# Optimization experiments

Measured on AMD Instinct MI355X. Metric: run time of the kernel, lower is better.

The kernel has to match this reference:

```python
import jax, jax.numpy as jnp
import numpy as np

EPS = 1e-9  # Dice BatchNormalization epsilon


def dice(x, alpha):
    # Keras BatchNormalization(axis=-1, center=False, scale=False) in training
    # mode: normalize over all axes except the last using batch statistics.
    mean = jnp.mean(x, axis=(0, 1), keepdims=True)
    var = jnp.var(x, axis=(0, 1), keepdims=True)
    x_normed = (x - mean) * jax.lax.rsqrt(var + EPS)
    p = jax.nn.sigmoid(x_normed)
    return alpha * (1.0 - p) * x + p * x


def setup_inputs() -> dict:
    key = jax.random.key(0)
    ks = jax.random.split(key, 11)
    B, T, D = 512, 2048, 20
    keys_ = jax.random.normal(ks[0], (B, T, D), dtype=jnp.float32)
    query = jax.random.normal(ks[1], (B, 1, D), dtype=jnp.float32)
    mask = jax.random.randint(ks[2], (B, T), 0, 2) > 0
    # DNN tower weights: hidden dims 80 -> 32 -> 16, attention head 16 -> 1
    W0 = jax.random.normal(ks[3], (80, 32), dtype=jnp.float32) * 0.1
    b0 = jax.random.normal(ks[4], (32,), dtype=jnp.float32) * 0.1
    a0 = jax.random.normal(ks[5], (32,), dtype=jnp.float32) * 0.1
    W1 = jax.random.normal(ks[6], (32, 16), dtype=jnp.float32) * 0.1
    b1 = jax.random.normal(ks[7], (16,), dtype=jnp.float32) * 0.1
    a1 = jax.random.normal(ks[8], (16,), dtype=jnp.float32) * 0.1
    wk = jax.random.normal(ks[9], (16, 1), dtype=jnp.float32) * 0.1
    bk = jax.random.normal(ks[10], (1,), dtype=jnp.float32) * 0.1
    return {"keys": keys_, "query": query, "mask": mask,
            "W0": W0, "b0": b0, "a0": a0,
            "W1": W1, "b1": b1, "a1": a1,
            "wk": wk, "bk": bk}


def reference(keys, query, mask, W0, b0, a0, W1, b1, a1, wk, bk):
    B, T, D = keys.shape
    # repeat query along the key/time axis: [B,1,D] -> [B,T,D]
    queries = jnp.broadcast_to(query, (B, T, D))
    # local-activation features: [B,T,4D] = [B,T,80]
    att = jnp.concatenate([queries, keys, queries - keys, queries * keys], axis=-1)
    # DNN tower with Dice activations (dropout is identity at inference)
    h = dice(att @ W0 + b0, a0)   # [B,T,32]
    h = dice(h @ W1 + b1, a1)     # [B,T,16]
    score = h @ wk + bk           # [B,T,1]
    outputs = jnp.transpose(score, (0, 2, 1))  # [B,1,T]
    # NOTE: the original code computes the masked scores into self.outputs but
    # then (weight_normalization=False, return_score=False) overwrites it with
    # matmul(outputs, keys) using the UNMASKED scores -- we reproduce that.
    return jnp.matmul(outputs, keys)  # [B,1,D]
```

## Files before the change

### kernel.cpp

```cpp
#include <hip/hip_runtime.h>


#define BB 512
#define TT 2048
#define DD 20
#define C0 32
#define C1 16

#define NTH 256
#define NPOS 4
#define POSB (NTH * NPOS)
#define NSLOT 8

#define WS_P1 0
#define WS_P2 512
#define WS_SCALE0 768
#define WS_SHIFT0 800
#define WS_SCALE1 832
#define WS_SHIFT1 848
#define WS_ZERO_N 768
#define WS_BLOB 896
#define BLOB_J 24
#define BLOB_B (C0 * BLOB_J)

#define PIN(x) asm volatile("" : "+v"(x))

__device__ __forceinline__ float fast_sigmoid(float x) {
    return __builtin_amdgcn_rcpf(1.0f + __expf(-x));
}

__device__ __forceinline__ void load_krow(const float* __restrict__ row,
                                          float* kk) {
    const float4* kr = (const float4*)row;
    float4 a = kr[0], b = kr[1], c = kr[2], d = kr[3], e = kr[4];
    kk[0] = a.x; kk[1] = a.y; kk[2] = a.z; kk[3] = a.w;
    kk[4] = b.x; kk[5] = b.y; kk[6] = b.z; kk[7] = b.w;
    kk[8] = c.x; kk[9] = c.y; kk[10] = c.z; kk[11] = c.w;
    kk[12] = d.x; kk[13] = d.y; kk[14] = d.z; kk[15] = d.w;
    kk[16] = e.x; kk[17] = e.y; kk[18] = e.z; kk[19] = e.w;
}

__global__ void prep_kernel(const float* __restrict__ query,
                            const float* __restrict__ W0,
                            const float* __restrict__ b0,
                            float* __restrict__ blob) {
    const int b = blockIdx.x * 2 + (threadIdx.x >> 5);
    const int j = threadIdx.x & 31;
    float cj = b0[j];
    float* dst = blob + (size_t)b * BLOB_B + j * BLOB_J;
#pragma unroll
    for (int d = 0; d < DD; ++d) {
        float w_q = W0[d * C0 + j];
        float w_k = W0[(DD + d) * C0 + j];
        float w_d = W0[(2 * DD + d) * C0 + j];
        float w_p = W0[(3 * DD + d) * C0 + j];
        float qd = query[b * DD + d];
        dst[d] = w_k - w_d + qd * w_p;
        cj = fmaf(qd, w_q + w_d, cj);
    }
    dst[20] = cj;
}

__global__ __launch_bounds__(NTH, 2) void pass1_kernel(
    const float* __restrict__ keys, const float* __restrict__ blob,
    float* __restrict__ sums) {
    const int b = blockIdx.x;
    const int tid = threadIdx.x, lane = tid & 63;
    const float* bA = blob + (size_t)b * BLOB_B;
    const float* kbase = keys + (size_t)b * TT * DD;

    float s[C0], q[C0];
#pragma unroll
    for (int j = 0; j < C0; ++j) { s[j] = 0.f; q[j] = 0.f; }

#pragma unroll 1
    for (int r = 0; r < TT / POSB; ++r) {
        float kk[NPOS][DD];
#pragma unroll
        for (int pp = 0; pp < NPOS; ++pp)
            load_krow(kbase + (size_t)(r * POSB + tid + pp * NTH) * DD,
                      kk[pp]);
#pragma unroll
        for (int pp = 0; pp < NPOS; ++pp)
#pragma unroll
            for (int d = 0; d < DD; ++d) PIN(kk[pp][d]);
#pragma unroll
        for (int j = 0; j < C0; ++j) {
            const float* wr = bA + j * BLOB_J;
            const float cj = wr[20];
            float sv = 0.f, qv = 0.f;
#pragma unroll
            for (int pp = 0; pp < NPOS; ++pp) {
                float hh = cj;
#pragma unroll
                for (int d = 0; d < DD; ++d)
                    hh = fmaf(kk[pp][d], wr[d], hh);
                sv += hh;
                qv = fmaf(hh, hh, qv);
            }
            s[j] += sv;
            q[j] += qv;
        }
    }
    float redv = 0.f;
#pragma unroll
    for (int v = 0; v < 2 * C0; ++v) {
        float val = (v < C0) ? s[v] : q[v - C0];
#pragma unroll
        for (int o = 32; o >= 1; o >>= 1) val += __shfl_xor(val, o);
        if (lane == v) redv = val;
    }
    atomicAdd(&sums[WS_P1 + (blockIdx.x & (NSLOT - 1)) * (2 * C0) + lane],
              redv);
}

__global__ void finalize_kernel(float* __restrict__ ws, int nch, int srcOff,
                                int scOff, int shOff) {
    int j = threadIdx.x;
    if (j < nch) {
        float s = 0.f, q = 0.f;
#pragma unroll
        for (int k = 0; k < NSLOT; ++k) {
            s += ws[srcOff + k * 2 * nch + j];
            q += ws[srcOff + k * 2 * nch + nch + j];
        }
        const float invN = 1.0f / (float)(BB * TT);
        float mean = s * invN;
        float var = q * invN - mean * mean;
        float scv = rsqrtf(var + 1e-9f);
        ws[scOff + j] = scv;
        ws[shOff + j] = -mean * scv;
    }
}

#define LOAD_AND_PIN_KEYS()                                                  \
    const float* kbase = keys + ((size_t)b * TT + chunk * POSB) * DD;        \
    float kk[NPOS][DD];                                                      \
    _Pragma("unroll") for (int pp = 0; pp < NPOS; ++pp)                      \
        load_krow(kbase + (size_t)(tid + pp * NTH) * DD, kk[pp]);            \
    _Pragma("unroll") for (int pp = 0; pp < NPOS; ++pp)                      \
        _Pragma("unroll") for (int d = 0; d < DD; ++d) PIN(kk[pp][d]);

#define TOWER_JLOOP()                                                        \
    _Pragma("unroll 1") for (int j = 0; j < C0; ++j) {                       \
        const float* wr = bA + j * BLOB_J;                                   \
        const float* ur = W1 + j * C1;                                       \
        const float cj = wr[20];                                             \
        const float sc = stats[WS_SCALE0 + j];                               \
        const float sh = stats[WS_SHIFT0 + j];                               \
        const float al = a0[j];                                              \
        const float nal = 1.0f - al;                                         \
        float h[NPOS];                                                       \
        _Pragma("unroll") for (int pp = 0; pp < NPOS; ++pp) {                \
            float hh = cj;                                                   \
            _Pragma("unroll") for (int d = 0; d < DD; ++d)                   \
                hh = fmaf(kk[pp][d], wr[d], hh);                             \
            h[pp] = hh;                                                      \
        }                                                                    \
        _Pragma("unroll") for (int pp = 0; pp < NPOS; ++pp) {                \
            float pr = fast_sigmoid(fmaf(h[pp], sc, sh));                    \
            float h0d = h[pp] * fmaf(pr, nal, al);                           \
            _Pragma("unroll") for (int c = 0; c < C1; ++c)                   \
                h1[pp][c] = fmaf(h0d, ur[c], h1[pp][c]);                     \
        }                                                                    \
    }

__global__ __launch_bounds__(NTH, 2) void pass2_kernel(
    const float* __restrict__ keys, const float* __restrict__ blob,
    const float* __restrict__ a0, const float* __restrict__ W1,
    const float* __restrict__ b1, const float* __restrict__ stats,
    float* __restrict__ sums) {
    const int b = blockIdx.x >> 1, chunk = blockIdx.x & 1;
    const int tid = threadIdx.x, lane = tid & 63;
    const float* bA = blob + (size_t)b * BLOB_B;

    LOAD_AND_PIN_KEYS()

    float h1[NPOS][C1];
#pragma unroll
    for (int pp = 0; pp < NPOS; ++pp)
#pragma unroll
        for (int c = 0; c < C1; ++c) h1[pp][c] = 0.f;

    TOWER_JLOOP()

    float s1[C1], q1[C1];
#pragma unroll
    for (int c = 0; c < C1; ++c) {
        float bc = b1[c], sv = 0.f, qv = 0.f;
#pragma unroll
        for (int pp = 0; pp < NPOS; ++pp) {
            float v = h1[pp][c] + bc;
            sv += v;
            qv = fmaf(v, v, qv);
        }
        s1[c] = sv;
        q1[c] = qv;
    }
    float redv = 0.f;
#pragma unroll
    for (int v = 0; v < 2 * C1; ++v) {
        float val = (v < C1) ? s1[v] : q1[v - C1];
#pragma unroll
        for (int o = 32; o >= 1; o >>= 1) val += __shfl_xor(val, o);
        if (lane == v) redv = val;
    }
    if (lane < 2 * C1)
        atomicAdd(&sums[WS_P2 + (blockIdx.x & (NSLOT - 1)) * (2 * C1) + lane],
                  redv);
}

__global__ __launch_bounds__(NTH, 2) void pass3_kernel(
    const float* __restrict__ keys, const float* __restrict__ blob,
    const float* __restrict__ a0, const float* __restrict__ W1,
    const float* __restrict__ b1, const float* __restrict__ a1,
    const float* __restrict__ wk, const float* __restrict__ bk,
    const float* __restrict__ stats, float* __restrict__ out) {
    const int b = blockIdx.x >> 1, chunk = blockIdx.x & 1;
    const int tid = threadIdx.x, lane = tid & 63;
    const float* bA = blob + (size_t)b * BLOB_B;

    LOAD_AND_PIN_KEYS()

    float h1[NPOS][C1];
#pragma unroll
    for (int pp = 0; pp < NPOS; ++pp)
#pragma unroll
        for (int c = 0; c < C1; ++c) h1[pp][c] = 0.f;

    TOWER_JLOOP()

    const float bkv = bk[0];
    float oacc[DD];
#pragma unroll
    for (int d = 0; d < DD; ++d) oacc[d] = 0.f;
#pragma unroll
    for (int pp = 0; pp < NPOS; ++pp) {
        float score = bkv;
#pragma unroll
        for (int c = 0; c < C1; ++c) {
            float v = h1[pp][c] + b1[c];
            float pr = fast_sigmoid(
                fmaf(v, stats[WS_SCALE1 + c], stats[WS_SHIFT1 + c]));
            float al = a1[c];
            float hd = v * fmaf(pr, 1.0f - al, al);
            score = fmaf(hd, wk[c], score);
        }
#pragma unroll
        for (int d = 0; d < DD; ++d)
            oacc[d] = fmaf(score, kk[pp][d], oacc[d]);
    }
    float redv = 0.f;
#pragma unroll
    for (int v = 0; v < DD; ++v) {
        float val = oacc[v];
#pragma unroll
        for (int o = 32; o >= 1; o >>= 1) val += __shfl_xor(val, o);
        if (lane == v) redv = val;
    }
    if (lane < DD) atomicAdd(&out[b * DD + lane], redv);
}

extern "C" void kernel_launch(void* const* d_in, const int* in_sizes, int n_in,
                              void* d_out, int out_size, void* d_ws,
                              size_t ws_size, hipStream_t stream) {
    const float* keys = (const float*)d_in[0];
    const float* query = (const float*)d_in[1];
    const float* W0 = (const float*)d_in[3];
    const float* b0 = (const float*)d_in[4];
    const float* a0 = (const float*)d_in[5];
    const float* W1 = (const float*)d_in[6];
    const float* b1 = (const float*)d_in[7];
    const float* a1 = (const float*)d_in[8];
    const float* wk = (const float*)d_in[9];
    const float* bk = (const float*)d_in[10];
    float* out = (float*)d_out;
    float* ws = (float*)d_ws;
    float* blob = ws + WS_BLOB;

    hipMemsetAsync(ws, 0, WS_ZERO_N * sizeof(float), stream);
    hipMemsetAsync(out, 0, (size_t)out_size * sizeof(float), stream);

    prep_kernel<<<BB / 2, 64, 0, stream>>>(query, W0, b0, blob);

    pass1_kernel<<<BB, NTH, 0, stream>>>(keys, blob, ws);
    finalize_kernel<<<1, 32, 0, stream>>>(ws, C0, WS_P1, WS_SCALE0, WS_SHIFT0);
    pass2_kernel<<<BB * 2, NTH, 0, stream>>>(keys, blob, a0, W1, b1, ws, ws);
    finalize_kernel<<<1, 16, 0, stream>>>(ws, C1, WS_P2, WS_SCALE1, WS_SHIFT1);
    pass3_kernel<<<BB * 2, NTH, 0, stream>>>(keys, blob, a0, W1, b1, a1, wk,
                                             bk, ws, out);
}
```

Baseline: 279.9 us.

## Fuse three passes into one cooperative kernel with grid-wide syncs

Replaces the pass1/finalize/pass2/finalize/pass3 launch chain with a single cooperative kernel of one block per batch row. Grid-wide syncs separate the statistics phases, and each block finalizes the BN statistics into shared memory itself. The output is written directly after a block-level reduction, so the output memset and the atomics go away. Each block now walks all 2048 positions in every phase, which halves the grid for passes 2 and 3. The cooperative launch also needs all 512 blocks to be co-resident, with a fallback to separate kernels when they are not.

```diff
diff --git a/kernel.cpp b/kernel.cpp
--- a/kernel.cpp
+++ b/kernel.cpp
@@ -1,4 +1,7 @@
 #include <hip/hip_runtime.h>
+#include <hip/hip_cooperative_groups.h>
+
+namespace cg = cooperative_groups;
 
 
 #define BB 512
@@ -10,20 +13,19 @@
 #define NTH 256
 #define NPOS 4
 #define POSB (NTH * NPOS)
+#define NROUND (TT / POSB)
 #define NSLOT 8
 
 #define WS_P1 0
 #define WS_P2 512
-#define WS_SCALE0 768
-#define WS_SHIFT0 800
-#define WS_SCALE1 832
-#define WS_SHIFT1 848
 #define WS_ZERO_N 768
 #define WS_BLOB 896
 #define BLOB_J 24
 #define BLOB_B (C0 * BLOB_J)
 
 #define PIN(x) asm volatile("" : "+v"(x))
+#define AGLOAD(p) \
+    __hip_atomic_load((p), __ATOMIC_RELAXED, __HIP_MEMORY_SCOPE_AGENT)
 
 __device__ __forceinline__ float fast_sigmoid(float x) {
     return __builtin_amdgcn_rcpf(1.0f + __expf(-x));
@@ -61,83 +63,10 @@
     dst[20] = cj;
 }
 
-__global__ __launch_bounds__(NTH, 2) void pass1_kernel(
-    const float* __restrict__ keys, const float* __restrict__ blob,
-    float* __restrict__ sums) {
-    const int b = blockIdx.x;
-    const int tid = threadIdx.x, lane = tid & 63;
-    const float* bA = blob + (size_t)b * BLOB_B;
-    const float* kbase = keys + (size_t)b * TT * DD;
-
-    float s[C0], q[C0];
-#pragma unroll
-    for (int j = 0; j < C0; ++j) { s[j] = 0.f; q[j] = 0.f; }
-
-#pragma unroll 1
-    for (int r = 0; r < TT / POSB; ++r) {
-        float kk[NPOS][DD];
-#pragma unroll
-        for (int pp = 0; pp < NPOS; ++pp)
-            load_krow(kbase + (size_t)(r * POSB + tid + pp * NTH) * DD,
-                      kk[pp]);
-#pragma unroll
-        for (int pp = 0; pp < NPOS; ++pp)
-#pragma unroll
-            for (int d = 0; d < DD; ++d) PIN(kk[pp][d]);
-#pragma unroll
-        for (int j = 0; j < C0; ++j) {
-            const float* wr = bA + j * BLOB_J;
-            const float cj = wr[20];
-            float sv = 0.f, qv = 0.f;
-#pragma unroll
-            for (int pp = 0; pp < NPOS; ++pp) {
-                float hh = cj;
-#pragma unroll
-                for (int d = 0; d < DD; ++d)
-                    hh = fmaf(kk[pp][d], wr[d], hh);
-                sv += hh;
-                qv = fmaf(hh, hh, qv);
-            }
-            s[j] += sv;
-            q[j] += qv;
-        }
-    }
-    float redv = 0.f;
-#pragma unroll
-    for (int v = 0; v < 2 * C0; ++v) {
-        float val = (v < C0) ? s[v] : q[v - C0];
-#pragma unroll
-        for (int o = 32; o >= 1; o >>= 1) val += __shfl_xor(val, o);
-        if (lane == v) redv = val;
-    }
-    atomicAdd(&sums[WS_P1 + (blockIdx.x & (NSLOT - 1)) * (2 * C0) + lane],
-              redv);
-}
-
-__global__ void finalize_kernel(float* __restrict__ ws, int nch, int srcOff,
-                                int scOff, int shOff) {
-    int j = threadIdx.x;
-    if (j < nch) {
-        float s = 0.f, q = 0.f;
-#pragma unroll
-        for (int k = 0; k < NSLOT; ++k) {
-            s += ws[srcOff + k * 2 * nch + j];
-            q += ws[srcOff + k * 2 * nch + nch + j];
-        }
-        const float invN = 1.0f / (float)(BB * TT);
-        float mean = s * invN;
-        float var = q * invN - mean * mean;
-        float scv = rsqrtf(var + 1e-9f);
-        ws[scOff + j] = scv;
-        ws[shOff + j] = -mean * scv;
-    }
-}
-
-#define LOAD_AND_PIN_KEYS()                                                  \
-    const float* kbase = keys + ((size_t)b * TT + chunk * POSB) * DD;        \
+#define LOAD_AND_PIN_KEYS(r)                                                 \
     float kk[NPOS][DD];                                                      \
     _Pragma("unroll") for (int pp = 0; pp < NPOS; ++pp)                      \
-        load_krow(kbase + (size_t)(tid + pp * NTH) * DD, kk[pp]);            \
+        load_krow(kbase + (size_t)((r)*POSB + tid + pp * NTH) * DD, kk[pp]); \
     _Pragma("unroll") for (int pp = 0; pp < NPOS; ++pp)                      \
         _Pragma("unroll") for (int d = 0; d < DD; ++d) PIN(kk[pp][d]);
 
@@ -146,8 +75,7 @@
         const float* wr = bA + j * BLOB_J;                                   \
         const float* ur = W1 + j * C1;                                       \
         const float cj = wr[20];                                             \
-        const float sc = stats[WS_SCALE0 + j];                               \
-        const float sh = stats[WS_SHIFT0 + j];                               \
+        const float2 ss = lss0[j];                                           \
         const float al = a0[j];                                              \
         const float nal = 1.0f - al;                                         \
         float h[NPOS];                                                       \
@@ -158,56 +86,225 @@
             h[pp] = hh;                                                      \
         }                                                                    \
         _Pragma("unroll") for (int pp = 0; pp < NPOS; ++pp) {                \
-            float pr = fast_sigmoid(fmaf(h[pp], sc, sh));                    \
+            float pr = fast_sigmoid(fmaf(h[pp], ss.x, ss.y));                \
             float h0d = h[pp] * fmaf(pr, nal, al);                           \
             _Pragma("unroll") for (int c = 0; c < C1; ++c)                   \
                 h1[pp][c] = fmaf(h0d, ur[c], h1[pp][c]);                     \
         }                                                                    \
     }
 
+__device__ __forceinline__ void phase1_body(int b, int tid, int lane,
+                                            const float* __restrict__ bA,
+                                            const float* __restrict__ kbase,
+                                            float* __restrict__ ws) {
+    float s[C0], q[C0];
+#pragma unroll
+    for (int j = 0; j < C0; ++j) { s[j] = 0.f; q[j] = 0.f; }
+#pragma unroll 1
+    for (int r = 0; r < NROUND; ++r) {
+        LOAD_AND_PIN_KEYS(r)
+#pragma unroll
+        for (int j = 0; j < C0; ++j) {
+            const float* wr = bA + j * BLOB_J;
+            const float cj = wr[20];
+            float sv = 0.f, qv = 0.f;
+#pragma unroll
+            for (int pp = 0; pp < NPOS; ++pp) {
+                float hh = cj;
+#pragma unroll
+                for (int d = 0; d < DD; ++d) hh = fmaf(kk[pp][d], wr[d], hh);
+                sv += hh;
+                qv = fmaf(hh, hh, qv);
+            }
+            s[j] += sv;
+            q[j] += qv;
+        }
+    }
+    float redv = 0.f;
+#pragma unroll
+    for (int v = 0; v < 2 * C0; ++v) {
+        float val = (v < C0) ? s[v] : q[v - C0];
+#pragma unroll
+        for (int o = 32; o >= 1; o >>= 1) val += __shfl_xor(val, o);
+        if (lane == v) redv = val;
+    }
+    atomicAdd(&ws[WS_P1 + (b & (NSLOT - 1)) * (2 * C0) + lane], redv);
+}
+
+__device__ __forceinline__ void finalize0(int tid, float* __restrict__ ws,
+                                          float2* __restrict__ lss0) {
+    if (tid < C0) {
+        float sv = 0.f, qv = 0.f;
+#pragma unroll
+        for (int k = 0; k < NSLOT; ++k) {
+            sv += AGLOAD(&ws[WS_P1 + k * (2 * C0) + tid]);
+            qv += AGLOAD(&ws[WS_P1 + k * (2 * C0) + C0 + tid]);
+        }
+        const float invN = 1.0f / (float)(BB * TT);
+        float mean = sv * invN;
+        float var = qv * invN - mean * mean;
+        float sc = rsqrtf(var + 1e-9f);
+        lss0[tid] = make_float2(sc, -mean * sc);
+    }
+}
+
+__device__ __forceinline__ void phase2_body(
+    int b, int tid, int lane, const float* __restrict__ bA,
+    const float* __restrict__ kbase, const float* __restrict__ a0,
+    const float* __restrict__ W1, const float* __restrict__ b1,
+    const float2* __restrict__ lss0, float* __restrict__ ws) {
+    float s1[C1], q1[C1];
+#pragma unroll
+    for (int c = 0; c < C1; ++c) { s1[c] = 0.f; q1[c] = 0.f; }
+#pragma unroll 1
+    for (int r = 0; r < NROUND; ++r) {
+        LOAD_AND_PIN_KEYS(r)
+        float h1[NPOS][C1];
+#pragma unroll
+        for (int pp = 0; pp < NPOS; ++pp)
+#pragma unroll
+            for (int c = 0; c < C1; ++c) h1[pp][c] = 0.f;
+        TOWER_JLOOP()
+#pragma unroll
+        for (int c = 0; c < C1; ++c) {
+            float bc = b1[c];
+#pragma unroll
+            for (int pp = 0; pp < NPOS; ++pp) {
+                float v = h1[pp][c] + bc;
+                s1[c] += v;
+                q1[c] = fmaf(v, v, q1[c]);
+            }
+        }
+    }
+    float redv = 0.f;
+#pragma unroll
+    for (int v = 0; v < 2 * C1; ++v) {
+        float val = (v < C1) ? s1[v] : q1[v - C1];
+#pragma unroll
+        for (int o = 32; o >= 1; o >>= 1) val += __shfl_xor(val, o);
+        if (lane == v) redv = val;
+    }
+    if (lane < 2 * C1)
+        atomicAdd(&ws[WS_P2 + (b & (NSLOT - 1)) * (2 * C1) + lane], redv);
+}
+
+__device__ __forceinline__ void finalize1(int tid, float* __restrict__ ws,
+                                          const float* __restrict__ a1,
+                                          const float* __restrict__ wk,
+                                          float4* __restrict__ ld1v) {
+    if (tid < C1) {
+        float sv = 0.f, qv = 0.f;
+#pragma unroll
+        for (int k = 0; k < NSLOT; ++k) {
+            sv += AGLOAD(&ws[WS_P2 + k * (2 * C1) + tid]);
+            qv += AGLOAD(&ws[WS_P2 + k * (2 * C1) + C1 + tid]);
+        }
+        const float invN = 1.0f / (float)(BB * TT);
+        float mean = sv * invN;
+        float var = qv * invN - mean * mean;
+        float sc = rsqrtf(var + 1e-9f);
+        ld1v[tid] = make_float4(sc, -mean * sc, a1[tid], wk[tid]);
+    }
+}
+
+__device__ __forceinline__ void phase3_body(
+    int b, int tid, int lane, int wave, const float* __restrict__ bA,
+    const float* __restrict__ kbase, const float* __restrict__ a0,
+    const float* __restrict__ W1, const float* __restrict__ b1,
+    const float* __restrict__ bk, const float2* __restrict__ lss0,
+    const float4* __restrict__ ld1v, float (*red)[DD],
+    float* __restrict__ out) {
+    const float bkv = bk[0];
+    float oacc[DD];
+#pragma unroll
+    for (int d = 0; d < DD; ++d) oacc[d] = 0.f;
+#pragma unroll 1
+    for (int r = 0; r < NROUND; ++r) {
+        LOAD_AND_PIN_KEYS(r)
+        float h1[NPOS][C1];
+#pragma unroll
+        for (int pp = 0; pp < NPOS; ++pp)
+#pragma unroll
+            for (int c = 0; c < C1; ++c) h1[pp][c] = 0.f;
+        TOWER_JLOOP()
+#pragma unroll
+        for (int pp = 0; pp < NPOS; ++pp) {
+            float score = bkv;
+#pragma unroll
+            for (int c = 0; c < C1; ++c) {
+                float v = h1[pp][c] + b1[c];
+                float4 dv = ld1v[c];
+                float pr = fast_sigmoid(fmaf(v, dv.x, dv.y));
+                float hd = v * fmaf(pr, 1.0f - dv.z, dv.z);
+                score = fmaf(hd, dv.w, score);
+            }
+#pragma unroll
+            for (int d = 0; d < DD; ++d)
+                oacc[d] = fmaf(score, kk[pp][d], oacc[d]);
+        }
+    }
+    float redv = 0.f;
+#pragma unroll
+    for (int v = 0; v < DD; ++v) {
+        float val = oacc[v];
+#pragma unroll
+        for (int o = 32; o >= 1; o >>= 1) val += __shfl_xor(val, o);
+        if (lane == v) redv = val;
+    }
+    if (lane < DD) red[wave][lane] = redv;
+    __syncthreads();
+    if (tid < DD)
+        out[b * DD + tid] =
+            red[0][tid] + red[1][tid] + red[2][tid] + red[3][tid];
+}
+
+__global__ __launch_bounds__(NTH, 2) void fused_kernel(
+    const float* __restrict__ keys, const float* __restrict__ blob,
+    const float* __restrict__ a0, const float* __restrict__ W1,
+    const float* __restrict__ b1, const float* __restrict__ a1,
+    const float* __restrict__ wk, const float* __restrict__ bk,
+    float* __restrict__ ws, float* __restrict__ out) {
+    const int b = blockIdx.x;
+    const int tid = threadIdx.x, wave = tid >> 6, lane = tid & 63;
+    const float* bA = blob + (size_t)b * BLOB_B;
+    const float* kbase = keys + (size_t)b * TT * DD;
+
+    __shared__ float2 lss0[C0];
+    __shared__ float4 ld1v[C1];
+    __shared__ float red[4][DD];
+
+    phase1_body(b, tid, lane, bA, kbase, ws);
+    cg::this_grid().sync();
+    finalize0(tid, ws, lss0);
+    __syncthreads();
+    phase2_body(b, tid, lane, bA, kbase, a0, W1, b1, lss0, ws);
+    cg::this_grid().sync();
+    finalize1(tid, ws, a1, wk, ld1v);
+    __syncthreads();
+    phase3_body(b, tid, lane, wave, bA, kbase, a0, W1, b1, bk, lss0, ld1v,
+                red, out);
+}
+
+__global__ __launch_bounds__(NTH, 2) void pass1_kernel(
+    const float* __restrict__ keys, const float* __restrict__ blob,
+    float* __restrict__ ws) {
+    const int b = blockIdx.x;
+    const int tid = threadIdx.x, lane = tid & 63;
+    phase1_body(b, tid, lane, blob + (size_t)b * BLOB_B,
+                keys + (size_t)b * TT * DD, ws);
+}
+
 __global__ __launch_bounds__(NTH, 2) void pass2_kernel(
     const float* __restrict__ keys, const float* __restrict__ blob,
     const float* __restrict__ a0, const float* __restrict__ W1,
-    const float* __restrict__ b1, const float* __restrict__ stats,
-    float* __restrict__ sums) {
-    const int b = blockIdx.x >> 1, chunk = blockIdx.x & 1;
+    const float* __restrict__ b1, float* __restrict__ ws) {
+    const int b = blockIdx.x;
     const int tid = threadIdx.x, lane = tid & 63;
-    const float* bA = blob + (size_t)b * BLOB_B;
-
-    LOAD_AND_PIN_KEYS()
-
-    float h1[NPOS][C1];
-#pragma unroll
-    for (int pp = 0; pp < NPOS; ++pp)
-#pragma unroll
-        for (int c = 0; c < C1; ++c) h1[pp][c] = 0.f;
-
-    TOWER_JLOOP()
-
-    float s1[C1], q1[C1];
-#pragma unroll
-    for (int c = 0; c < C1; ++c) {
-        float bc = b1[c], sv = 0.f, qv = 0.f;
-#pragma unroll
-        for (int pp = 0; pp < NPOS; ++pp) {
-            float v = h1[pp][c] + bc;
-            sv += v;
-            qv = fmaf(v, v, qv);
-        }
-        s1[c] = sv;
-        q1[c] = qv;
-    }
-    float redv = 0.f;
-#pragma unroll
-    for (int v = 0; v < 2 * C1; ++v) {
-        float val = (v < C1) ? s1[v] : q1[v - C1];
-#pragma unroll
-        for (int o = 32; o >= 1; o >>= 1) val += __shfl_xor(val, o);
-        if (lane == v) redv = val;
-    }
-    if (lane < 2 * C1)
-        atomicAdd(&sums[WS_P2 + (blockIdx.x & (NSLOT - 1)) * (2 * C1) + lane],
-                  redv);
+    __shared__ float2 lss0[C0];
+    finalize0(tid, ws, lss0);
+    __syncthreads();
+    phase2_body(b, tid, lane, blob + (size_t)b * BLOB_B,
+                keys + (size_t)b * TT * DD, a0, W1, b1, lss0, ws);
 }
 
 __global__ __launch_bounds__(NTH, 2) void pass3_kernel(
@@ -215,50 +312,18 @@
     const float* __restrict__ a0, const float* __restrict__ W1,
     const float* __restrict__ b1, const float* __restrict__ a1,
     const float* __restrict__ wk, const float* __restrict__ bk,
-    const float* __restrict__ stats, float* __restrict__ out) {
-    const int b = blockIdx.x >> 1, chunk = blockIdx.x & 1;
-    const int tid = threadIdx.x, lane = tid & 63;
-    const float* bA = blob + (size_t)b * BLOB_B;
-
-    LOAD_AND_PIN_KEYS()
-
-    float h1[NPOS][C1];
-#pragma unroll
-    for (int pp = 0; pp < NPOS; ++pp)
-#pragma unroll
-        for (int c = 0; c < C1; ++c) h1[pp][c] = 0.f;
-
-    TOWER_JLOOP()
-
-    const float bkv = bk[0];
-    float oacc[DD];
-#pragma unroll
-    for (int d = 0; d < DD; ++d) oacc[d] = 0.f;
-#pragma unroll
-    for (int pp = 0; pp < NPOS; ++pp) {
-        float score = bkv;
-#pragma unroll
-        for (int c = 0; c < C1; ++c) {
-            float v = h1[pp][c] + b1[c];
-            float pr = fast_sigmoid(
-                fmaf(v, stats[WS_SCALE1 + c], stats[WS_SHIFT1 + c]));
-            float al = a1[c];
-            float hd = v * fmaf(pr, 1.0f - al, al);
-            score = fmaf(hd, wk[c], score);
-        }
-#pragma unroll
-        for (int d = 0; d < DD; ++d)
-            oacc[d] = fmaf(score, kk[pp][d], oacc[d]);
-    }
-    float redv = 0.f;
-#pragma unroll
-    for (int v = 0; v < DD; ++v) {
-        float val = oacc[v];
-#pragma unroll
-        for (int o = 32; o >= 1; o >>= 1) val += __shfl_xor(val, o);
-        if (lane == v) redv = val;
-    }
-    if (lane < DD) atomicAdd(&out[b * DD + lane], redv);
+    float* __restrict__ ws, float* __restrict__ out) {
+    const int b = blockIdx.x;
+    const int tid = threadIdx.x, wave = tid >> 6, lane = tid & 63;
+    __shared__ float2 lss0[C0];
+    __shared__ float4 ld1v[C1];
+    __shared__ float red[4][DD];
+    finalize0(tid, ws, lss0);
+    finalize1(tid, ws, a1, wk, ld1v);
+    __syncthreads();
+    phase3_body(b, tid, lane, wave, blob + (size_t)b * BLOB_B,
+                keys + (size_t)b * TT * DD, a0, W1, b1, bk, lss0, ld1v, red,
+                out);
 }
 
 extern "C" void kernel_launch(void* const* d_in, const int* in_sizes, int n_in,
@@ -277,16 +342,36 @@
     float* out = (float*)d_out;
     float* ws = (float*)d_ws;
     float* blob = ws + WS_BLOB;
+    const float* blobc = blob;
 
     hipMemsetAsync(ws, 0, WS_ZERO_N * sizeof(float), stream);
-    hipMemsetAsync(out, 0, (size_t)out_size * sizeof(float), stream);
-
     prep_kernel<<<BB / 2, 64, 0, stream>>>(query, W0, b0, blob);
 
-    pass1_kernel<<<BB, NTH, 0, stream>>>(keys, blob, ws);
-    finalize_kernel<<<1, 32, 0, stream>>>(ws, C0, WS_P1, WS_SCALE0, WS_SHIFT0);
-    pass2_kernel<<<BB * 2, NTH, 0, stream>>>(keys, blob, a0, W1, b1, ws, ws);
-    finalize_kernel<<<1, 16, 0, stream>>>(ws, C1, WS_P2, WS_SCALE1, WS_SHIFT1);
-    pass3_kernel<<<BB * 2, NTH, 0, stream>>>(keys, blob, a0, W1, b1, a1, wk,
+    static int use_coop = -1;
+    if (use_coop < 0) {
+        int nb = 0, ncu = 0;
+        hipError_t e1 = hipOccupancyMaxActiveBlocksPerMultiprocessor(
+            &nb, (const void*)fused_kernel, NTH, 0);
+        hipDeviceProp_t prop;
+        hipError_t e2 = hipGetDeviceProperties(&prop, 0);
+        if (e2 == hipSuccess) ncu = prop.multiProcessorCount;
+        use_coop = (e1 == hipSuccess && e2 == hipSuccess && nb * ncu >= BB)
+                       ? 1
+                       : 0;
+    }
+
+    if (use_coop) {
+        void* args[] = {(void*)&keys, (void*)&blobc, (void*)&a0, (void*)&W1,
+                        (void*)&b1,   (void*)&a1,    (void*)&wk, (void*)&bk,
+                        (void*)&ws,   (void*)&out};
+        hipError_t e = hipLaunchCooperativeKernel(
+            (const void*)fused_kernel, dim3(BB), dim3(NTH), args, 0, stream);
+        if (e != hipSuccess) use_coop = 0;
+    }
+    if (!use_coop) {
+        pass1_kernel<<<BB, NTH, 0, stream>>>(keys, blob, ws);
+        pass2_kernel<<<BB, NTH, 0, stream>>>(keys, blob, a0, W1, b1, ws);
+        pass3_kernel<<<BB, NTH, 0, stream>>>(keys, blob, a0, W1, b1, a1, wk,
                                              bk, ws, out);
-}
+    }
+}
```

New measurement: 274.0 us. 1.02x faster.
